# Performance work log

Hardware: AMD Instinct MI355X
Metric: run time of the kernel (lower is better)

Reference implementation:

```python
import jax, jax.numpy as jnp
import numpy as np

N_NODES = 50000


def _segment_mean(vals, seg_ids, num_segments):
    s = jax.ops.segment_sum(vals, seg_ids, num_segments=num_segments)
    cnt = jax.ops.segment_sum(jnp.ones((vals.shape[0],), vals.dtype), seg_ids,
                              num_segments=num_segments)
    return s / jnp.clip(cnt, 1.0)[:, None]


def _sage_layer(h, src, dst, W_self, W_neigh, b):
    # mean-aggregate neighbor messages: gather h[src], scatter-mean to dst
    neigh = _segment_mean(h[src], dst, N_NODES)
    return h @ W_self + neigh @ W_neigh + b


def _edge_score(h, src, dst, Wp, bp):
    # concat(h_u, h_v) @ Wp == h_u @ Wp[:d] + h_v @ Wp[d:]
    d = h.shape[1]
    return h[src] @ Wp[:d] + h[dst] @ Wp[d:] + bp


def setup_inputs() -> dict:
    key = jax.random.key(0)
    ks = jax.random.split(key, 16)
    N, E, EP, EN = N_NODES, 800000, 200000, 200000
    d_in, d_hid, d_out = 128, 256, 128
    inp = {
        'x': jax.random.normal(ks[0], (N, d_in), jnp.float32),
        'msg_src': jax.random.randint(ks[1], (E,), 0, N, jnp.int32),
        'msg_dst': jax.random.randint(ks[2], (E,), 0, N, jnp.int32),
        'pos_src': jax.random.randint(ks[3], (EP,), 0, N, jnp.int32),
        'pos_dst': jax.random.randint(ks[4], (EP,), 0, N, jnp.int32),
        'neg_src': jax.random.randint(ks[5], (EN,), 0, N, jnp.int32),
        'neg_dst': jax.random.randint(ks[6], (EN,), 0, N, jnp.int32),
        'W1_self': jax.random.normal(ks[7], (d_in, d_hid), jnp.float32) * 0.05,
        'W1_neigh': jax.random.normal(ks[8], (d_in, d_hid), jnp.float32) * 0.05,
        'b1': jnp.zeros((d_hid,), jnp.float32),
        'W2_self': jax.random.normal(ks[9], (d_hid, d_out), jnp.float32) * 0.05,
        'W2_neigh': jax.random.normal(ks[10], (d_hid, d_out), jnp.float32) * 0.05,
        'b2': jnp.zeros((d_out,), jnp.float32),
        'Wp': jax.random.normal(ks[11], (2 * d_out, 1), jnp.float32) * 0.05,
        'bp': jnp.zeros((1,), jnp.float32),
    }
    return inp


def reference(x, msg_src, msg_dst, pos_src, pos_dst, neg_src, neg_dst,
              W1_self, W1_neigh, b1, W2_self, W2_neigh, b2, Wp, bp):
    h = _sage_layer(x, msg_src, msg_dst, W1_self, W1_neigh, b1)
    h = jax.nn.relu(h)
    h = _sage_layer(h, msg_src, msg_dst, W2_self, W2_neigh, b2)
    pos_score = _edge_score(h, pos_src, pos_dst, Wp, bp)
    neg_score = _edge_score(h, neg_src, neg_dst, Wp, bp)
    return pos_score, neg_score
```

## Files before the change

### kernel.cpp

```cpp
#include <hip/hip_runtime.h>


#define NN 50000
#define EM 800000
#define EPOS 200000
#define ENEG 200000
#define NB 196
#define CAP 8192
#define RPB 4096
#define CBLK 196
#define MTILES 3125
#define GEMM_GRID 512
#define XCONV 6250

typedef __bf16 bf16;
typedef bf16 bf16x4 __attribute__((ext_vector_type(4)));
typedef bf16 bf16x8 __attribute__((ext_vector_type(8)));
typedef float floatx4 __attribute__((ext_vector_type(4)));

#define I_CCUR 0
#define I_ROW  256
#define I_REND 50432
#define I_CSR  100608
#define B_CREG 6824960
#define B_XB   13247488
#define B_AGG1 26047488
#define B_H1   38847488
#define B_NV   64447488
#define B_WT1  65247488
#define B_WT2  65378560
#define B_P    65509632
#define B_Q    65710336

__global__ __launch_bounds__(256) void convbin_kernel(
    const float* __restrict__ x, bf16* __restrict__ xb,
    const float* __restrict__ W1s, const float* __restrict__ W1n,
    const float* __restrict__ W2n, const float* __restrict__ W2s,
    bf16* __restrict__ Wt1, bf16* __restrict__ Wt2,
    const int* __restrict__ msrc, const int* __restrict__ mdst,
    int* __restrict__ ccur, unsigned* __restrict__ creg) {
    if (blockIdx.x < XCONV) {
        int i = blockIdx.x * 256 + threadIdx.x;
        float4 v = ((const float4*)x)[i];
        bf16x4 o;
        o[0] = (bf16)v.x; o[1] = (bf16)v.y; o[2] = (bf16)v.z; o[3] = (bf16)v.w;
        *(bf16x4*)(xb + (size_t)i * 4) = o;
    } else if (blockIdx.x < XCONV + 256) {
        int i = (blockIdx.x - XCONV) * 256 + threadIdx.x;
        int n = i >> 8, k = i & 255;
        float w1 = (k < 128) ? W1s[k * 256 + n] : W1n[(k - 128) * 256 + n];
        Wt1[i] = (bf16)w1;
        float w2 = (n < 128) ? W2n[k * 128 + n] : W2s[k * 128 + (n - 128)];
        Wt2[i] = (bf16)w2;
    } else {
        __shared__ int hist[NB];
        __shared__ int cnt2[NB];
        __shared__ int goff[NB];
        __shared__ int base[256];
        __shared__ unsigned sorted[RPB];
        __shared__ unsigned char sbkt[RPB];
        int t = threadIdx.x;
        int cb = blockIdx.x - (XCONV + 256);
        int e0 = cb * RPB;
        int nrec = EM - e0; if (nrec > RPB) nrec = RPB;

        for (int i = t; i < NB; i += 256) { hist[i] = 0; cnt2[i] = 0; }
        __syncthreads();

        int myb[16];
        unsigned myrec[16];
#pragma unroll
        for (int j = 0; j < 16; ++j) {
            int idx = j * 256 + t;
            if (idx < nrec) {
                int s = msrc[e0 + idx], d = mdst[e0 + idx];
                myb[j] = d >> 8;
                myrec[j] = ((unsigned)(d & 255) << 16) | (unsigned)s;
                atomicAdd(&hist[myb[j]], 1);
            } else myb[j] = -1;
        }
        __syncthreads();

        base[t] = (t < NB) ? hist[t] : 0;
        __syncthreads();
        for (int o = 1; o < 256; o <<= 1) {
            int u = (t >= o) ? base[t - o] : 0;
            __syncthreads();
            base[t] += u;
            __syncthreads();
        }

        if (t < NB && hist[t] > 0)
            goff[t] = t * CAP + atomicAdd(&ccur[t], hist[t]);
#pragma unroll
        for (int j = 0; j < 16; ++j) {
            if (myb[j] >= 0) {
                int rk = atomicAdd(&cnt2[myb[j]], 1);
                int slot = base[myb[j]] - hist[myb[j]] + rk;
                sorted[slot] = myrec[j];
                sbkt[slot] = (unsigned char)myb[j];
            }
        }
        __syncthreads();

#pragma unroll
        for (int j = 0; j < 16; ++j) {
            int idx = j * 256 + t;
            if (idx < nrec) {
                int b = sbkt[idx];
                int exb = base[b] - hist[b];
                creg[(size_t)goff[b] + (idx - exb)] = sorted[idx];
            }
        }
    }
}

__global__ __launch_bounds__(256) void binsort_kernel(
    const unsigned* __restrict__ creg, const int* __restrict__ ccur,
    int* __restrict__ rowstart, int* __restrict__ rowend,
    int* __restrict__ csr) {
    __shared__ int lcnt[256];
    __shared__ int sc[256];
    __shared__ int lcur[256];
    int b = blockIdx.x, t = threadIdx.x;
    int beg = b * CAP;
    int cnt = ccur[b];
    lcnt[t] = 0;
    __syncthreads();
    for (int i = t; i < cnt; i += 256)
        atomicAdd(&lcnt[(int)(creg[beg + i] >> 16) & 255], 1);
    __syncthreads();
    sc[t] = lcnt[t];
    __syncthreads();
    for (int o = 1; o < 256; o <<= 1) {
        int u = (t >= o) ? sc[t - o] : 0;
        __syncthreads();
        sc[t] += u;
        __syncthreads();
    }
    int node = b * 256 + t;
    if (node < NN) {
        rowstart[node] = beg + sc[t] - lcnt[t];
        rowend[node] = beg + sc[t];
    }
    lcur[t] = beg + sc[t] - lcnt[t];
    __syncthreads();
    for (int i = t; i < cnt; i += 256) {
        unsigned rec = creg[beg + i];
        int pos = atomicAdd(&lcur[(int)(rec >> 16) & 255], 1);
        csr[pos] = (int)(rec & 0xffffu);
    }
}

__global__ __launch_bounds__(256) void gather1_kernel(const bf16* __restrict__ feat,
                                                      const int* __restrict__ rowstart,
                                                      const int* __restrict__ rowend,
                                                      const int* __restrict__ csr,
                                                      bf16* __restrict__ agg) {
    int node = (blockIdx.x * 256 + threadIdx.x) >> 6;
    if (node >= NN) return;
    int lane = threadIdx.x & 63;
    int q = lane >> 4, r = lane & 15;
    int c = r * 8;
    int beg = rowstart[node], end = rowend[node];
    float acc[8] = {0.f, 0.f, 0.f, 0.f, 0.f, 0.f, 0.f, 0.f};
    float acc2[8] = {0.f, 0.f, 0.f, 0.f, 0.f, 0.f, 0.f, 0.f};
    int i = beg + q;
    for (; i + 4 < end; i += 8) {
        int s0 = csr[i], s1 = csr[i + 4];
        bf16x8 v0 = *(const bf16x8*)(feat + (size_t)s0 * 128 + c);
        bf16x8 v1 = *(const bf16x8*)(feat + (size_t)s1 * 128 + c);
#pragma unroll
        for (int u = 0; u < 8; ++u) {
            acc[u] += (float)v0[u];
            acc2[u] += (float)v1[u];
        }
    }
    if (i < end) {
        int s0 = csr[i];
        bf16x8 v0 = *(const bf16x8*)(feat + (size_t)s0 * 128 + c);
#pragma unroll
        for (int u = 0; u < 8; ++u) acc[u] += (float)v0[u];
    }
#pragma unroll
    for (int u = 0; u < 8; ++u) acc[u] += acc2[u];
#pragma unroll
    for (int m = 16; m <= 32; m <<= 1)
#pragma unroll
        for (int u = 0; u < 8; ++u) acc[u] += __shfl_xor(acc[u], m);
    if (q == 0) {
        int deg = end - beg;
        float inv = 1.0f / (float)(deg > 0 ? deg : 1);
        bf16x8 o;
#pragma unroll
        for (int u = 0; u < 8; ++u) o[u] = (bf16)(acc[u] * inv);
        *(bf16x8*)(agg + (size_t)node * 128 + c) = o;
    }
}

__global__ __launch_bounds__(256) void gemm1_kernel(
    const bf16* __restrict__ xb, const bf16* __restrict__ aggb,
    const bf16* __restrict__ Wt, const float* __restrict__ b1,
    bf16* __restrict__ h1b) {
    int w = threadIdx.x >> 6;
    int lane = threadIdx.x & 63;
    int r = lane & 15, quad = lane >> 4;
    int colbase = w * 64;

    bf16x8 bfr[4][8];
#pragma unroll
    for (int t = 0; t < 4; ++t)
#pragma unroll
        for (int kk = 0; kk < 8; ++kk)
            bfr[t][kk] = *(const bf16x8*)(Wt + (size_t)(colbase + t * 16 + r) * 256
                                          + kk * 32 + quad * 8);
    float bb[4];
#pragma unroll
    for (int t = 0; t < 4; ++t) bb[t] = b1[colbase + t * 16 + r];

    for (int tile = blockIdx.x; tile < MTILES; tile += GEMM_GRID) {
        int m0 = tile * 16;
        int row = m0 + r;
        bf16x8 a[8];
#pragma unroll
        for (int kk = 0; kk < 4; ++kk)
            a[kk] = *(const bf16x8*)(xb + (size_t)row * 128 + kk * 32 + quad * 8);
#pragma unroll
        for (int kk = 4; kk < 8; ++kk)
            a[kk] = *(const bf16x8*)(aggb + (size_t)row * 128 + (kk - 4) * 32 + quad * 8);
        floatx4 acc[4];
#pragma unroll
        for (int t = 0; t < 4; ++t) acc[t] = (floatx4){0.f, 0.f, 0.f, 0.f};
#pragma unroll
        for (int kk = 0; kk < 8; ++kk)
#pragma unroll
            for (int t = 0; t < 4; ++t)
                acc[t] = __builtin_amdgcn_mfma_f32_16x16x32_bf16(a[kk], bfr[t][kk],
                                                                 acc[t], 0, 0, 0);
        int mb = m0 + quad * 4;
#pragma unroll
        for (int t = 0; t < 4; ++t) {
            int col = colbase + t * 16 + r;
#pragma unroll
            for (int rr = 0; rr < 4; ++rr) {
                float v = acc[t][rr] + bb[t];
                v = v > 0.f ? v : 0.f;
                h1b[(size_t)(mb + rr) * 256 + col] = (bf16)v;
            }
        }
    }
}

__global__ __launch_bounds__(256) void gemm2_kernel(
    const bf16* __restrict__ h1b, const bf16* __restrict__ Wt,
    const float* __restrict__ b2, const float* __restrict__ wp,
    float4* __restrict__ nodev) {
    __shared__ float lp[4][16];
    __shared__ float lq[4][16];
    int w = threadIdx.x >> 6;
    int lane = threadIdx.x & 63;
    int r = lane & 15, quad = lane >> 4;
    int colbase = w * 64;

    bf16x8 bfr[4][8];
#pragma unroll
    for (int t = 0; t < 4; ++t)
#pragma unroll
        for (int kk = 0; kk < 8; ++kk)
            bfr[t][kk] = *(const bf16x8*)(Wt + (size_t)(colbase + t * 16 + r) * 256
                                          + kk * 32 + quad * 8);
    float bb[4], wA[4], wB[4];
#pragma unroll
    for (int t = 0; t < 4; ++t) {
        int col = colbase + t * 16 + r;
        if (w < 2) {
            bb[t] = 0.f;
            wA[t] = wp[col];
            wB[t] = wp[128 + col];
        } else {
            int c2 = col - 128;
            bb[t] = b2[c2];
            wA[t] = wp[c2];
            wB[t] = wp[128 + c2];
        }
    }

    for (int tile = blockIdx.x; tile < MTILES; tile += GEMM_GRID) {
        int m0 = tile * 16;
        int row = m0 + r;
        bf16x8 a[8];
#pragma unroll
        for (int kk = 0; kk < 8; ++kk)
            a[kk] = *(const bf16x8*)(h1b + (size_t)row * 256 + kk * 32 + quad * 8);
        floatx4 acc[4];
#pragma unroll
        for (int t = 0; t < 4; ++t) acc[t] = (floatx4){0.f, 0.f, 0.f, 0.f};
#pragma unroll
        for (int kk = 0; kk < 8; ++kk)
#pragma unroll
            for (int t = 0; t < 4; ++t)
                acc[t] = __builtin_amdgcn_mfma_f32_16x16x32_bf16(a[kk], bfr[t][kk],
                                                                 acc[t], 0, 0, 0);
        float pacc[4], qacc[4];
#pragma unroll
        for (int rr = 0; rr < 4; ++rr) {
            float pr = 0.f, qr = 0.f;
#pragma unroll
            for (int t = 0; t < 4; ++t) {
                float v = acc[t][rr] + bb[t];
                pr += v * wA[t];
                qr += v * wB[t];
            }
            pacc[rr] = pr;
            qacc[rr] = qr;
        }
#pragma unroll
        for (int m = 1; m <= 8; m <<= 1) {
#pragma unroll
            for (int rr = 0; rr < 4; ++rr) {
                pacc[rr] += __shfl_xor(pacc[rr], m);
                qacc[rr] += __shfl_xor(qacc[rr], m);
            }
        }
        if (r == 0) {
#pragma unroll
            for (int rr = 0; rr < 4; ++rr) {
                lp[w][quad * 4 + rr] = pacc[rr];
                lq[w][quad * 4 + rr] = qacc[rr];
            }
        }
        __syncthreads();
        if (threadIdx.x < 16) {
            int rw = threadIdx.x;
            float4 o;
            o.x = lp[0][rw] + lp[1][rw];
            o.y = lq[0][rw] + lq[1][rw];
            o.z = lp[2][rw] + lp[3][rw];
            o.w = lq[2][rw] + lq[3][rw];
            nodev[m0 + rw] = o;
        }
        __syncthreads();
    }
}

__global__ __launch_bounds__(256) void gather2_kernel(
    const float4* __restrict__ nodev, const int* __restrict__ rowstart,
    const int* __restrict__ rowend, const int* __restrict__ csr,
    float* __restrict__ p, float* __restrict__ q) {
    int t = threadIdx.x;
    int node = blockIdx.x * 16 + (t >> 4);
    if (node >= NN) return;
    int l = t & 15;
    int beg = rowstart[node], end = rowend[node];
    float pz = 0.f, qz = 0.f;
    for (int i = beg + l; i < end; i += 16) {
        float4 v = nodev[csr[i]];
        pz += v.x;
        qz += v.y;
    }
#pragma unroll
    for (int m = 8; m >= 1; m >>= 1) {
        pz += __shfl_xor(pz, m);
        qz += __shfl_xor(qz, m);
    }
    if (l == 0) {
        int deg = end - beg;
        float inv = 1.0f / (float)(deg > 0 ? deg : 1);
        float4 me = nodev[node];
        p[node] = me.z + pz * inv;
        q[node] = me.w + qz * inv;
    }
}

__global__ __launch_bounds__(256) void score_kernel(
    const int* __restrict__ psrc, const int* __restrict__ pdst,
    const int* __restrict__ nsrc, const int* __restrict__ ndst,
    const float* __restrict__ p, const float* __restrict__ q,
    const float* __restrict__ bp, float* __restrict__ out) {
    int i = blockIdx.x * blockDim.x + threadIdx.x;
    float b = bp[0];
    if (i < EPOS) {
        out[i] = p[psrc[i]] + q[pdst[i]] + b;
    } else if (i < EPOS + ENEG) {
        int j = i - EPOS;
        out[i] = p[nsrc[j]] + q[ndst[j]] + b;
    }
}

extern "C" void kernel_launch(void* const* d_in, const int* in_sizes, int n_in,
                              void* d_out, int out_size, void* d_ws, size_t ws_size,
                              hipStream_t stream) {
    const float* x    = (const float*)d_in[0];
    const int*   msrc = (const int*)d_in[1];
    const int*   mdst = (const int*)d_in[2];
    const int*   psrc = (const int*)d_in[3];
    const int*   pdst = (const int*)d_in[4];
    const int*   nsrc = (const int*)d_in[5];
    const int*   ndst = (const int*)d_in[6];
    const float* W1s  = (const float*)d_in[7];
    const float* W1n  = (const float*)d_in[8];
    const float* b1   = (const float*)d_in[9];
    const float* W2s  = (const float*)d_in[10];
    const float* W2n  = (const float*)d_in[11];
    const float* b2   = (const float*)d_in[12];
    const float* wp   = (const float*)d_in[13];
    const float* bp   = (const float*)d_in[14];

    char* ws = (char*)d_ws;
    int*   ccur     = (int*)ws + I_CCUR;
    int*   rowstart = (int*)ws + I_ROW;
    int*   rowend   = (int*)ws + I_REND;
    int*   csr      = (int*)ws + I_CSR;
    unsigned* creg  = (unsigned*)(ws + B_CREG);
    bf16*  xb    = (bf16*)(ws + B_XB);
    bf16*  agg1b = (bf16*)(ws + B_AGG1);
    bf16*  h1b   = (bf16*)(ws + B_H1);
    float4* nodev = (float4*)(ws + B_NV);
    bf16*  Wt1   = (bf16*)(ws + B_WT1);
    bf16*  Wt2   = (bf16*)(ws + B_WT2);
    float* p     = (float*)(ws + B_P);
    float* q     = (float*)(ws + B_Q);
    float* out   = (float*)d_out;

    hipMemsetAsync(ccur, 0, NB * sizeof(int), stream);

    convbin_kernel<<<XCONV + 256 + CBLK, 256, 0, stream>>>(
        x, xb, W1s, W1n, W2n, W2s, Wt1, Wt2, msrc, mdst, ccur, creg);
    binsort_kernel<<<NB, 256, 0, stream>>>(creg, ccur, rowstart, rowend, csr);

    gather1_kernel<<<(NN + 3) / 4, 256, 0, stream>>>(xb, rowstart, rowend, csr, agg1b);
    gemm1_kernel<<<GEMM_GRID, 256, 0, stream>>>(xb, agg1b, Wt1, b1, h1b);
    gemm2_kernel<<<GEMM_GRID, 256, 0, stream>>>(h1b, Wt2, b2, wp, nodev);
    gather2_kernel<<<(NN + 15) / 16, 256, 0, stream>>>(nodev, rowstart, rowend, csr, p, q);
    score_kernel<<<(EPOS + ENEG + 255) / 256, 256, 0, stream>>>(
        psrc, pdst, nsrc, ndst, p, q, bp, out);
}
```

Before: 218.9 us.

## Fuse bucket CSR build with layer-1 gather and drop global atomic binning

The binning stage now writes each block's locally sorted records contiguously, along with per-bucket count and offset matrices, so it no longer needs global atomics on bucket cursors or the memset that cleared them. A new 1024-thread bucket kernel collects each bucket's pieces from all blocks into shared memory and builds that bucket's CSR rows. In the same kernel it performs the layer-1 mean gather, reading neighbor indices from LDS. This removes one launch, the global atomics and the re-read of csr for the first gather. The cost is that the gather now runs on only 196 large blocks with heavy shared memory use, which may reduce parallelism.

After: 215.2 us. No clear change (-1.7%).

```diff
diff --git a/kernel.cpp b/kernel.cpp
--- a/kernel.cpp
+++ b/kernel.cpp
@@ -12,25 +12,27 @@
 #define MTILES 3125
 #define GEMM_GRID 512
 #define XCONV 6250
+#define BT 1024
 
 typedef __bf16 bf16;
 typedef bf16 bf16x4 __attribute__((ext_vector_type(4)));
 typedef bf16 bf16x8 __attribute__((ext_vector_type(8)));
 typedef float floatx4 __attribute__((ext_vector_type(4)));
 
-#define I_CCUR 0
-#define I_ROW  256
-#define I_REND 50432
-#define I_CSR  100608
-#define B_CREG 6824960
-#define B_XB   13247488
-#define B_AGG1 26047488
-#define B_H1   38847488
-#define B_NV   64447488
-#define B_WT1  65247488
-#define B_WT2  65378560
-#define B_P    65509632
-#define B_Q    65710336
+#define I_CNT  0
+#define I_OFF  38416
+#define I_ROW  76832
+#define I_REND 127008
+#define I_CSR  177184
+#define B_CREG 7131264
+#define B_XB   10331264
+#define B_AGG1 23131264
+#define B_H1   35931264
+#define B_NV   61531264
+#define B_WT1  62331264
+#define B_WT2  62462336
+#define B_P    62593408
+#define B_Q    62793408
 
 __global__ __launch_bounds__(256) void convbin_kernel(
     const float* __restrict__ x, bf16* __restrict__ xb,
@@ -38,7 +40,8 @@
     const float* __restrict__ W2n, const float* __restrict__ W2s,
     bf16* __restrict__ Wt1, bf16* __restrict__ Wt2,
     const int* __restrict__ msrc, const int* __restrict__ mdst,
-    int* __restrict__ ccur, unsigned* __restrict__ creg) {
+    unsigned* __restrict__ creg, int* __restrict__ cntM,
+    int* __restrict__ offM) {
     if (blockIdx.x < XCONV) {
         int i = blockIdx.x * 256 + threadIdx.x;
         float4 v = ((const float4*)x)[i];
@@ -55,10 +58,8 @@
     } else {
         __shared__ int hist[NB];
         __shared__ int cnt2[NB];
-        __shared__ int goff[NB];
         __shared__ int base[256];
         __shared__ unsigned sorted[RPB];
-        __shared__ unsigned char sbkt[RPB];
         int t = threadIdx.x;
         int cb = blockIdx.x - (XCONV + 256);
         int e0 = cb * RPB;
@@ -90,111 +91,134 @@
             __syncthreads();
         }
 
-        if (t < NB && hist[t] > 0)
-            goff[t] = t * CAP + atomicAdd(&ccur[t], hist[t]);
 #pragma unroll
         for (int j = 0; j < 16; ++j) {
             if (myb[j] >= 0) {
                 int rk = atomicAdd(&cnt2[myb[j]], 1);
                 int slot = base[myb[j]] - hist[myb[j]] + rk;
                 sorted[slot] = myrec[j];
-                sbkt[slot] = (unsigned char)myb[j];
-            }
-        }
-        __syncthreads();
-
+            }
+        }
+        __syncthreads();
+
+        if (t < NB) {
+            cntM[t * CBLK + cb] = hist[t];
+            offM[t * CBLK + cb] = base[t] - hist[t];
+        }
 #pragma unroll
         for (int j = 0; j < 16; ++j) {
             int idx = j * 256 + t;
-            if (idx < nrec) {
-                int b = sbkt[idx];
-                int exb = base[b] - hist[b];
-                creg[(size_t)goff[b] + (idx - exb)] = sorted[idx];
-            }
-        }
-    }
-}
-
-__global__ __launch_bounds__(256) void binsort_kernel(
-    const unsigned* __restrict__ creg, const int* __restrict__ ccur,
-    int* __restrict__ rowstart, int* __restrict__ rowend,
-    int* __restrict__ csr) {
-    __shared__ int lcnt[256];
+            if (idx < nrec) creg[(size_t)cb * RPB + idx] = sorted[idx];
+        }
+    }
+}
+
+__global__ __launch_bounds__(1024) void bucket_kernel(
+    const unsigned* __restrict__ creg, const int* __restrict__ cntM,
+    const int* __restrict__ offM, int* __restrict__ rowstart,
+    int* __restrict__ rowend, int* __restrict__ csr,
+    const bf16* __restrict__ feat, bf16* __restrict__ agg) {
+    __shared__ unsigned lrec[CAP];
+    __shared__ unsigned lsrc[CAP];
+    __shared__ int ccnt[256];
+    __shared__ int cpos[256];
+    __shared__ int coff[256];
+    __shared__ int lhist[256];
     __shared__ int sc[256];
     __shared__ int lcur[256];
     int b = blockIdx.x, t = threadIdx.x;
-    int beg = b * CAP;
-    int cnt = ccur[b];
-    lcnt[t] = 0;
-    __syncthreads();
-    for (int i = t; i < cnt; i += 256)
-        atomicAdd(&lcnt[(int)(creg[beg + i] >> 16) & 255], 1);
-    __syncthreads();
-    sc[t] = lcnt[t];
+
+    if (t < 256) {
+        int cc = 0, oo = 0;
+        if (t < CBLK) { cc = cntM[b * CBLK + t]; oo = offM[b * CBLK + t]; }
+        ccnt[t] = cc; cpos[t] = cc; coff[t] = oo; lhist[t] = 0;
+    }
     __syncthreads();
     for (int o = 1; o < 256; o <<= 1) {
-        int u = (t >= o) ? sc[t - o] : 0;
-        __syncthreads();
-        sc[t] += u;
-        __syncthreads();
-    }
-    int node = b * 256 + t;
-    if (node < NN) {
-        rowstart[node] = beg + sc[t] - lcnt[t];
-        rowend[node] = beg + sc[t];
-    }
-    lcur[t] = beg + sc[t] - lcnt[t];
+        int u = (t < 256 && t >= o) ? cpos[t - o] : 0;
+        __syncthreads();
+        if (t < 256) cpos[t] += u;
+        __syncthreads();
+    }
+
+    int wid = t >> 6, lane = t & 63;
+    for (int cb = wid; cb < CBLK; cb += 16) {
+        int c = ccnt[cb], ofs = coff[cb], d0 = cpos[cb] - c;
+        for (int i = lane; i < c; i += 64) {
+            unsigned rec = creg[(size_t)cb * RPB + ofs + i];
+            lrec[d0 + i] = rec;
+            atomicAdd(&lhist[(int)(rec >> 16) & 255], 1);
+        }
+    }
     __syncthreads();
-    for (int i = t; i < cnt; i += 256) {
-        unsigned rec = creg[beg + i];
-        int pos = atomicAdd(&lcur[(int)(rec >> 16) & 255], 1);
-        csr[pos] = (int)(rec & 0xffffu);
-    }
-}
-
-__global__ __launch_bounds__(256) void gather1_kernel(const bf16* __restrict__ feat,
-                                                      const int* __restrict__ rowstart,
-                                                      const int* __restrict__ rowend,
-                                                      const int* __restrict__ csr,
-                                                      bf16* __restrict__ agg) {
-    int node = (blockIdx.x * 256 + threadIdx.x) >> 6;
-    if (node >= NN) return;
-    int lane = threadIdx.x & 63;
+    int cntb = cpos[255];
+
+    if (t < 256) sc[t] = lhist[t];
+    __syncthreads();
+    for (int o = 1; o < 256; o <<= 1) {
+        int u = (t < 256 && t >= o) ? sc[t - o] : 0;
+        __syncthreads();
+        if (t < 256) sc[t] += u;
+        __syncthreads();
+    }
+    if (t < 256) {
+        int node = b * 256 + t;
+        if (node < NN) {
+            rowstart[node] = b * CAP + sc[t] - lhist[t];
+            rowend[node] = b * CAP + sc[t];
+        }
+        lcur[t] = sc[t] - lhist[t];
+    }
+    __syncthreads();
+
+    for (int i = t; i < cntb; i += BT) {
+        unsigned rec = lrec[i];
+        int slot = atomicAdd(&lcur[(int)(rec >> 16) & 255], 1);
+        lsrc[slot] = rec & 0xffffu;
+    }
+    __syncthreads();
+    for (int i = t; i < cntb; i += BT) csr[b * CAP + i] = (int)lsrc[i];
+
     int q = lane >> 4, r = lane & 15;
-    int c = r * 8;
-    int beg = rowstart[node], end = rowend[node];
-    float acc[8] = {0.f, 0.f, 0.f, 0.f, 0.f, 0.f, 0.f, 0.f};
-    float acc2[8] = {0.f, 0.f, 0.f, 0.f, 0.f, 0.f, 0.f, 0.f};
-    int i = beg + q;
-    for (; i + 4 < end; i += 8) {
-        int s0 = csr[i], s1 = csr[i + 4];
-        bf16x8 v0 = *(const bf16x8*)(feat + (size_t)s0 * 128 + c);
-        bf16x8 v1 = *(const bf16x8*)(feat + (size_t)s1 * 128 + c);
-#pragma unroll
-        for (int u = 0; u < 8; ++u) {
-            acc[u] += (float)v0[u];
-            acc2[u] += (float)v1[u];
-        }
-    }
-    if (i < end) {
-        int s0 = csr[i];
-        bf16x8 v0 = *(const bf16x8*)(feat + (size_t)s0 * 128 + c);
-#pragma unroll
-        for (int u = 0; u < 8; ++u) acc[u] += (float)v0[u];
-    }
-#pragma unroll
-    for (int u = 0; u < 8; ++u) acc[u] += acc2[u];
-#pragma unroll
-    for (int m = 16; m <= 32; m <<= 1)
-#pragma unroll
-        for (int u = 0; u < 8; ++u) acc[u] += __shfl_xor(acc[u], m);
-    if (q == 0) {
-        int deg = end - beg;
-        float inv = 1.0f / (float)(deg > 0 ? deg : 1);
-        bf16x8 o;
-#pragma unroll
-        for (int u = 0; u < 8; ++u) o[u] = (bf16)(acc[u] * inv);
-        *(bf16x8*)(agg + (size_t)node * 128 + c) = o;
+    int cch = r * 8;
+    for (int k = 0; k < 16; ++k) {
+        int ln = wid * 16 + k;
+        int node = b * 256 + ln;
+        if (node >= NN) break;
+        int beg = sc[ln] - lhist[ln], end = sc[ln];
+        float acc[8] = {0.f, 0.f, 0.f, 0.f, 0.f, 0.f, 0.f, 0.f};
+        float acc2[8] = {0.f, 0.f, 0.f, 0.f, 0.f, 0.f, 0.f, 0.f};
+        int i = beg + q;
+        for (; i + 4 < end; i += 8) {
+            int s0 = (int)lsrc[i], s1 = (int)lsrc[i + 4];
+            bf16x8 v0 = *(const bf16x8*)(feat + (size_t)s0 * 128 + cch);
+            bf16x8 v1 = *(const bf16x8*)(feat + (size_t)s1 * 128 + cch);
+#pragma unroll
+            for (int u = 0; u < 8; ++u) {
+                acc[u] += (float)v0[u];
+                acc2[u] += (float)v1[u];
+            }
+        }
+        if (i < end) {
+            int s0 = (int)lsrc[i];
+            bf16x8 v0 = *(const bf16x8*)(feat + (size_t)s0 * 128 + cch);
+#pragma unroll
+            for (int u = 0; u < 8; ++u) acc[u] += (float)v0[u];
+        }
+#pragma unroll
+        for (int u = 0; u < 8; ++u) acc[u] += acc2[u];
+#pragma unroll
+        for (int m = 16; m <= 32; m <<= 1)
+#pragma unroll
+            for (int u = 0; u < 8; ++u) acc[u] += __shfl_xor(acc[u], m);
+        if (q == 0) {
+            int deg = end - beg;
+            float inv = 1.0f / (float)(deg > 0 ? deg : 1);
+            bf16x8 o;
+#pragma unroll
+            for (int u = 0; u < 8; ++u) o[u] = (bf16)(acc[u] * inv);
+            *(bf16x8*)(agg + (size_t)node * 128 + cch) = o;
+        }
     }
 }
 
@@ -407,7 +431,8 @@
     const float* bp   = (const float*)d_in[14];
 
     char* ws = (char*)d_ws;
-    int*   ccur     = (int*)ws + I_CCUR;
+    int*   cntM     = (int*)ws + I_CNT;
+    int*   offM     = (int*)ws + I_OFF;
     int*   rowstart = (int*)ws + I_ROW;
     int*   rowend   = (int*)ws + I_REND;
     int*   csr      = (int*)ws + I_CSR;
@@ -422,13 +447,10 @@
     float* q     = (float*)(ws + B_Q);
     float* out   = (float*)d_out;
 
-    hipMemsetAsync(ccur, 0, NB * sizeof(int), stream);
-
     convbin_kernel<<<XCONV + 256 + CBLK, 256, 0, stream>>>(
-        x, xb, W1s, W1n, W2n, W2s, Wt1, Wt2, msrc, mdst, ccur, creg);
-    binsort_kernel<<<NB, 256, 0, stream>>>(creg, ccur, rowstart, rowend, csr);
-
-    gather1_kernel<<<(NN + 3) / 4, 256, 0, stream>>>(xb, rowstart, rowend, csr, agg1b);
+        x, xb, W1s, W1n, W2n, W2s, Wt1, Wt2, msrc, mdst, creg, cntM, offM);
+    bucket_kernel<<<NB, BT, 0, stream>>>(creg, cntM, offM, rowstart, rowend,
+                                         csr, xb, agg1b);
     gemm1_kernel<<<GEMM_GRID, 256, 0, stream>>>(xb, agg1b, Wt1, b1, h1b);
     gemm2_kernel<<<GEMM_GRID, 256, 0, stream>>>(h1b, Wt2, b2, wp, nodev);
     gather2_kernel<<<(NN + 15) / 16, 256, 0, stream>>>(nodev, rowstart, rowend, csr, p, q);
```
